# Kernel tuning notes

Measured on AMD Instinct MI355X. Metric: run time of the kernel, lower is better.

Reference implementation:

```python
import jax, jax.numpy as jnp
import numpy as np

WS = 8  # window size
NH = 6  # num heads


def _rel_pos_index(ws):
    coords = jnp.stack(jnp.meshgrid(jnp.arange(ws), jnp.arange(ws), indexing='ij'))  # (2, ws, ws)
    cf = coords.reshape(2, -1)                      # (2, ws*ws)
    rel = cf[:, :, None] - cf[:, None, :]           # (2, ws2, ws2)
    return (rel[0] + ws - 1) * (2 * ws - 1) + (rel[1] + ws - 1)  # (ws2, ws2) int


def setup_inputs() -> dict:
    key = jax.random.key(0)
    k1, k2, k3, k4, k5 = jax.random.split(key, 5)
    B, H, W, C = 4, 256, 256, 192
    dim = C
    x = jax.random.normal(k1, (B, H * W, C), dtype=jnp.float32)
    qkv_w = jax.random.normal(k2, (3 * dim, dim), dtype=jnp.float32) * (dim ** -0.5)
    proj_w = jax.random.normal(k3, (dim, dim), dtype=jnp.float32) * (dim ** -0.5)
    proj_b = jax.random.normal(k4, (dim,), dtype=jnp.float32) * 0.01
    rpb_table = jax.random.normal(k5, ((2 * WS - 1) ** 2, NH), dtype=jnp.float32) * 0.02
    return {"x": x, "qkv_w": qkv_w, "proj_w": proj_w, "proj_b": proj_b,
            "rpb_table": rpb_table, "H": H, "W": W}


def reference(x, qkv_w, proj_w, proj_b, rpb_table, H, W):
    B, L, C = x.shape
    ws, nh = WS, NH
    hd = C // nh
    scale = hd ** -0.5
    ws2 = ws * ws

    pad_r = (ws - W % ws) % ws
    pad_b = (ws - H % ws) % ws
    Hp, Wp = H + pad_b, W + pad_r
    xi = x.reshape(B, H, W, C)
    if pad_r > 0 or pad_b > 0:
        xi = jnp.pad(xi, ((0, 0), (0, pad_b), (0, pad_r), (0, 0)))

    # window partition -> (nW, ws2, C)
    win = xi.reshape(B, Hp // ws, ws, Wp // ws, ws, C)
    win = win.transpose(0, 1, 3, 2, 4, 5).reshape(-1, ws2, C)

    # qkv projection (no bias)
    qkv = (win @ qkv_w.T).reshape(-1, ws2, 3, nh, hd)
    q = qkv[:, :, 0].transpose(0, 2, 1, 3) * scale  # (nW, nh, ws2, hd)
    k = qkv[:, :, 1].transpose(0, 2, 1, 3)
    v = qkv[:, :, 2].transpose(0, 2, 1, 3)

    attn = jnp.einsum('nhqd,nhkd->nhqk', q, k)      # (nW, nh, ws2, ws2)
    bias = rpb_table[_rel_pos_index(ws)]            # (ws2, ws2, nh)
    attn = attn + bias.transpose(2, 0, 1)[None]
    attn = jax.nn.softmax(attn, axis=-1)

    out = jnp.einsum('nhqk,nhkd->nhqd', attn, v)    # (nW, nh, ws2, hd)
    out = out.transpose(0, 2, 1, 3).reshape(-1, ws2, C)
    out = out @ proj_w.T + proj_b

    # window reverse
    xo = out.reshape(B, Hp // ws, Wp // ws, ws, ws, C)
    xo = xo.transpose(0, 1, 3, 2, 4, 5).reshape(B, Hp, Wp, C)
    if pad_r > 0 or pad_b > 0:
        xo = xo[:, :H, :W, :]
    return xo.reshape(B, H * W, C)
```

## Files before the change

### kernel.cpp

```cpp
#include <hip/hip_runtime.h>

typedef _Float16 f16;
typedef _Float16 f16x8 __attribute__((ext_vector_type(8)));
typedef _Float16 f16x4 __attribute__((ext_vector_type(4)));
typedef __fp16 h16x2 __attribute__((ext_vector_type(2)));
typedef float f32x4 __attribute__((ext_vector_type(4)));

constexpr int HDIM = 256, WDIM = 256, C_ = 192, NH_ = 6;
constexpr float SCALE = 0.17677669529663687f;
constexpr int XP = 200;

#define SCHED_FENCE() __builtin_amdgcn_sched_barrier(0)

constexpr size_t OFF_WQ   = 0;
constexpr size_t OFF_WP   = 221184;
constexpr size_t OFF_BIAS = 294912;

__global__ __launch_bounds__(256) void prep_kernel(const float* __restrict__ qkv_w,
                                                   const float* __restrict__ proj_w,
                                                   const float* __restrict__ rpb,
                                                   f16* __restrict__ wqp, f16* __restrict__ wpp,
                                                   f16* __restrict__ biasp) {
    int i = blockIdx.x * 256 + threadIdx.x;
    if (i < 13824) {
        int lane = i & 63, rest = i >> 6;
        int ks = rest % 6; rest /= 6;
        int dt = rest & 1; rest >>= 1;
        int c = rest % 3, w = rest / 3;
        int l15 = lane & 15, lg = lane >> 4;
        int row = c * 192 + w * 32 + dt * 16 + l15;
        int col = ks * 32 + lg * 8;
#pragma unroll
        for (int j = 0; j < 8; ++j) wqp[(size_t)i * 8 + j] = (f16)qkv_w[row * 192 + col + j];
    } else if (i < 18432) {
        int g = i - 13824;
        int lane = g & 63, rest = g >> 6;
        int ks = rest % 6; rest /= 6;
        int nt = rest & 1, w = rest >> 1;
        int l15 = lane & 15, lg = lane >> 4;
        int row = w * 32 + nt * 16 + l15;
        int col = ks * 32 + lg * 8;
#pragma unroll
        for (int j = 0; j < 8; ++j) wpp[(size_t)g * 8 + j] = (f16)proj_w[row * 192 + col + j];
    } else if (i < 24576) {
        int g = i - 18432;
        int lane = g & 63;
        int kt = (g >> 6) & 3, qt = (g >> 8) & 3, h = g >> 10;
        int q = qt * 16 + (lane & 15);
#pragma unroll
        for (int j = 0; j < 4; ++j) {
            int k = kt * 16 + (lane >> 4) * 4 + j;
            int dy = (q >> 3) - (k >> 3) + 7;
            int dx = (q & 7) - (k & 7) + 7;
            biasp[(size_t)g * 4 + j] = (f16)rpb[(dy * 15 + dx) * NH_ + h];
        }
    }
}

__global__ __launch_bounds__(128, 2) void fused_kernel(const float* __restrict__ x,
                                                       const f16* __restrict__ wqp,
                                                       const f16* __restrict__ wpp,
                                                       const float* __restrict__ pb,
                                                       const f16* __restrict__ biasp,
                                                       float* __restrict__ out) {
    __shared__ f16 xlds[64 * XP];
    const int tid = threadIdx.x;
    const int v = tid >> 6;
    const int lane = tid & 63;
    const int l15 = lane & 15, lg = lane >> 4;
    const int win = blockIdx.x;
    const int b = win >> 10, wy = (win >> 5) & 31, wx = win & 31;

#pragma unroll
    for (int it = 0; it < 24; ++it) {
        int u = tid + it * 128;
        int row = u / 48, c4 = u - row * 48;
        int gy = wy * 8 + (row >> 3), gx = wx * 8 + (row & 7);
        float4 vv = *((const float4*)(x + ((size_t)((b * HDIM + gy) * WDIM + gx)) * C_ + c4 * 4));
        h16x2 p0 = __builtin_amdgcn_cvt_pkrtz(vv.x, vv.y);
        h16x2 p1 = __builtin_amdgcn_cvt_pkrtz(vv.z, vv.w);
        f16x4 o4;
        o4[0] = (f16)p0[0]; o4[1] = (f16)p0[1]; o4[2] = (f16)p1[0]; o4[3] = (f16)p1[1];
        *((f16x4*)(xlds + row * XP + c4 * 4)) = o4;
    }
    SCHED_FENCE();
    __syncthreads();

    f16x4 oreg[3][4][2];

#pragma unroll
    for (int hh = 0; hh < 3; ++hh) {
        const int head = v * 3 + hh;
        const f16x8* wqb   = (const f16x8*)wqp + (size_t)head * 36 * 64 + lane;
        const f16x4* bbase = (const f16x4*)biasp + (size_t)head * 16 * 64 + lane;
        SCHED_FENCE();

        f16x4 qf[2][4], kf[2][4];
        {
            f32x4 aq[2][4], ak[2][4];
#pragma unroll
            for (int ii = 0; ii < 4; ++ii)
#pragma unroll
                for (int jj = 0; jj < 2; ++jj) {
                    f32x4 z = {0.f, 0.f, 0.f, 0.f};
                    aq[jj][ii] = z; ak[jj][ii] = z;
                }
#pragma unroll
            for (int ks = 0; ks < 6; ++ks) {
                f16x8 Wq0 = wqb[(size_t)(     ks) * 64], Wq1 = wqb[(size_t)( 6 + ks) * 64];
                f16x8 Wk0 = wqb[(size_t)(12 + ks) * 64], Wk1 = wqb[(size_t)(18 + ks) * 64];
#pragma unroll
                for (int tt = 0; tt < 4; ++tt) {
                    f16x8 xt = *((const f16x8*)(xlds + (tt * 16 + l15) * XP + ks * 32 + lg * 8));
                    aq[0][tt] = __builtin_amdgcn_mfma_f32_16x16x32_f16(Wq0, xt, aq[0][tt], 0, 0, 0);
                    aq[1][tt] = __builtin_amdgcn_mfma_f32_16x16x32_f16(Wq1, xt, aq[1][tt], 0, 0, 0);
                    ak[0][tt] = __builtin_amdgcn_mfma_f32_16x16x32_f16(Wk0, xt, ak[0][tt], 0, 0, 0);
                    ak[1][tt] = __builtin_amdgcn_mfma_f32_16x16x32_f16(Wk1, xt, ak[1][tt], 0, 0, 0);
                }
            }
#pragma unroll
            for (int dt = 0; dt < 2; ++dt)
#pragma unroll
                for (int tt = 0; tt < 4; ++tt)
#pragma unroll
                    for (int ii = 0; ii < 4; ++ii) {
                        qf[dt][tt][ii] = (f16)(aq[dt][tt][ii] * SCALE);
                        kf[dt][tt][ii] = (f16)(ak[dt][tt][ii]);
                    }
        }
        SCHED_FENCE();

        f16x4 vf[4][2];
        {
            f32x4 av[4][2];
#pragma unroll
            for (int ii = 0; ii < 4; ++ii)
#pragma unroll
                for (int jj = 0; jj < 2; ++jj) {
                    f32x4 z = {0.f, 0.f, 0.f, 0.f};
                    av[ii][jj] = z;
                }
#pragma unroll
            for (int ks = 0; ks < 6; ++ks) {
                f16x8 Wv0 = wqb[(size_t)(24 + ks) * 64], Wv1 = wqb[(size_t)(30 + ks) * 64];
#pragma unroll
                for (int tt = 0; tt < 4; ++tt) {
                    f16x8 xt = *((const f16x8*)(xlds + (tt * 16 + l15) * XP + ks * 32 + lg * 8));
                    av[tt][0] = __builtin_amdgcn_mfma_f32_16x16x32_f16(xt, Wv0, av[tt][0], 0, 0, 0);
                    av[tt][1] = __builtin_amdgcn_mfma_f32_16x16x32_f16(xt, Wv1, av[tt][1], 0, 0, 0);
                }
            }
#pragma unroll
            for (int tt = 0; tt < 4; ++tt)
#pragma unroll
                for (int dt = 0; dt < 2; ++dt)
#pragma unroll
                    for (int ii = 0; ii < 4; ++ii)
                        vf[tt][dt][ii] = (f16)(av[tt][dt][ii]);
        }
        SCHED_FENCE();

#pragma unroll
        for (int qt = 0; qt < 4; ++qt) {
            f16x4 bq[4];
#pragma unroll
            for (int kt = 0; kt < 4; ++kt)
                bq[kt] = bbase[(size_t)(qt * 4 + kt) * 64];
            f32x4 s[4];
#pragma unroll
            for (int kt = 0; kt < 4; ++kt) {
                f32x4 z = {0.f, 0.f, 0.f, 0.f};
                s[kt] = __builtin_amdgcn_mfma_f32_16x16x16f16(kf[0][kt], qf[0][qt], z, 0, 0, 0);
                s[kt] = __builtin_amdgcn_mfma_f32_16x16x16f16(kf[1][kt], qf[1][qt], s[kt], 0, 0, 0);
            }
#pragma unroll
            for (int kt = 0; kt < 4; ++kt)
#pragma unroll
                for (int ii = 0; ii < 4; ++ii) s[kt][ii] += (float)bq[kt][ii];

            float m = s[0][0];
#pragma unroll
            for (int kt = 0; kt < 4; ++kt)
#pragma unroll
                for (int ii = 0; ii < 4; ++ii) m = fmaxf(m, s[kt][ii]);
            m = fmaxf(m, __shfl_xor(m, 16));
            m = fmaxf(m, __shfl_xor(m, 32));
            float sum = 0.f;
            f16x4 pa[4];
#pragma unroll
            for (int kt = 0; kt < 4; ++kt)
#pragma unroll
                for (int ii = 0; ii < 4; ++ii) {
                    float e = __expf(s[kt][ii] - m);
                    sum += e;
                    pa[kt][ii] = (f16)e;
                }
            sum += __shfl_xor(sum, 16);
            sum += __shfl_xor(sum, 32);
            const float rq = 1.0f / sum;

#pragma unroll
            for (int dt = 0; dt < 2; ++dt) {
                f32x4 z = {0.f, 0.f, 0.f, 0.f};
                f32x4 o0 = __builtin_amdgcn_mfma_f32_16x16x16f16(vf[0][dt], pa[0], z, 0, 0, 0);
                o0 = __builtin_amdgcn_mfma_f32_16x16x16f16(vf[1][dt], pa[1], o0, 0, 0, 0);
                f32x4 o1 = __builtin_amdgcn_mfma_f32_16x16x16f16(vf[2][dt], pa[2], z, 0, 0, 0);
                o1 = __builtin_amdgcn_mfma_f32_16x16x16f16(vf[3][dt], pa[3], o1, 0, 0, 0);
                f32x4 o = o0 + o1;
                f16x4 ov;
#pragma unroll
                for (int ii = 0; ii < 4; ++ii) ov[ii] = (f16)(o[ii] * rq);
                oreg[hh][qt][dt] = ov;
            }
        }
    }
    SCHED_FENCE();
    __syncthreads();

#pragma unroll
    for (int hh = 0; hh < 3; ++hh) {
        const int head = v * 3 + hh;
#pragma unroll
        for (int qt = 0; qt < 4; ++qt)
#pragma unroll
            for (int dt = 0; dt < 2; ++dt)
                *((f16x4*)(xlds + (qt * 16 + l15) * XP + head * 32 + dt * 16 + lg * 4)) = oreg[hh][qt][dt];
    }
    SCHED_FENCE();
    __syncthreads();

#pragma unroll
    for (int hh = 0; hh < 3; ++hh) {
        const int head = v * 3 + hh;
        const f16x8* wpb = (const f16x8*)wpp + (size_t)head * 12 * 64 + lane;
#pragma unroll
        for (int nt = 0; nt < 2; ++nt) {
            f16x8 wpf[6];
#pragma unroll
            for (int ks = 0; ks < 6; ++ks)
                wpf[ks] = wpb[(size_t)(nt * 6 + ks) * 64];
            f32x4 bv = *((const f32x4*)(pb + head * 32 + nt * 16 + lg * 4));
#pragma unroll
            for (int qt = 0; qt < 4; ++qt) {
                f32x4 acc = {0.f, 0.f, 0.f, 0.f};
#pragma unroll
                for (int ks = 0; ks < 6; ++ks) {
                    f16x8 af = *((const f16x8*)(xlds + (qt * 16 + l15) * XP + ks * 32 + lg * 8));
                    acc = __builtin_amdgcn_mfma_f32_16x16x32_f16(wpf[ks], af, acc, 0, 0, 0);
                }
                acc += bv;
                const int t = qt * 16 + l15;
                const int gy = wy * 8 + (t >> 3), gx = wx * 8 + (t & 7);
                *((f32x4*)(out + ((size_t)((b * HDIM + gy) * WDIM + gx)) * C_ + head * 32 + nt * 16 + lg * 4)) = acc;
            }
        }
    }
}

extern "C" void kernel_launch(void* const* d_in, const int* in_sizes, int n_in,
                              void* d_out, int out_size, void* d_ws, size_t ws_size,
                              hipStream_t stream) {
    const float* x      = (const float*)d_in[0];
    const float* qkv_w  = (const float*)d_in[1];
    const float* proj_w = (const float*)d_in[2];
    const float* proj_b = (const float*)d_in[3];
    const float* rpb    = (const float*)d_in[4];
    float* out = (float*)d_out;
    char* ws = (char*)d_ws;
    f16* wqp   = (f16*)(ws + OFF_WQ);
    f16* wpp   = (f16*)(ws + OFF_WP);
    f16* biasp = (f16*)(ws + OFF_BIAS);

    prep_kernel<<<96, 256, 0, stream>>>(qkv_w, proj_w, rpb, wqp, wpp, biasp);
    fused_kernel<<<4096, 128, 0, stream>>>(x, wqp, wpp, proj_b, biasp, out);
}
```

Before: 172.6 us.

## Fold scale and log2e into weights, seed MFMA with fp32 bias, raise occupancy

Folds the attention scale and log2(e) into the Q weights and the relative-position bias during prep, so softmax can use raw v_exp_f32 and a hardware reciprocal. The bias is stored in fp32 and passed as the MFMA accumulator seed, which removes the separate bias add. Launch bounds go from 2 to 3 blocks per SIMD, and the x load loop is split into three scheduling groups. The higher occupancy target may force register spills, and the fp32 bias doubles that table's memory traffic.

```diff
diff --git a/kernel.cpp b/kernel.cpp
--- a/kernel.cpp
+++ b/kernel.cpp
@@ -8,6 +8,8 @@
 
 constexpr int HDIM = 256, WDIM = 256, C_ = 192, NH_ = 6;
 constexpr float SCALE = 0.17677669529663687f;
+constexpr float L2E = 1.4426950408889634f;
+constexpr float SCALE2 = SCALE * L2E;
 constexpr int XP = 200;
 
 #define SCHED_FENCE() __builtin_amdgcn_sched_barrier(0)
@@ -20,7 +22,7 @@
                                                    const float* __restrict__ proj_w,
                                                    const float* __restrict__ rpb,
                                                    f16* __restrict__ wqp, f16* __restrict__ wpp,
-                                                   f16* __restrict__ biasp) {
+                                                   float* __restrict__ biasp) {
     int i = blockIdx.x * 256 + threadIdx.x;
     if (i < 13824) {
         int lane = i & 63, rest = i >> 6;
@@ -30,8 +32,9 @@
         int l15 = lane & 15, lg = lane >> 4;
         int row = c * 192 + w * 32 + dt * 16 + l15;
         int col = ks * 32 + lg * 8;
-#pragma unroll
-        for (int j = 0; j < 8; ++j) wqp[(size_t)i * 8 + j] = (f16)qkv_w[row * 192 + col + j];
+        float sc = (c == 0) ? SCALE2 : 1.0f;
+#pragma unroll
+        for (int j = 0; j < 8; ++j) wqp[(size_t)i * 8 + j] = (f16)(qkv_w[row * 192 + col + j] * sc);
     } else if (i < 18432) {
         int g = i - 13824;
         int lane = g & 63, rest = g >> 6;
@@ -52,16 +55,16 @@
             int k = kt * 16 + (lane >> 4) * 4 + j;
             int dy = (q >> 3) - (k >> 3) + 7;
             int dx = (q & 7) - (k & 7) + 7;
-            biasp[(size_t)g * 4 + j] = (f16)rpb[(dy * 15 + dx) * NH_ + h];
+            biasp[(size_t)g * 4 + j] = rpb[(dy * 15 + dx) * NH_ + h] * L2E;
         }
     }
 }
 
-__global__ __launch_bounds__(128, 2) void fused_kernel(const float* __restrict__ x,
+__global__ __launch_bounds__(128, 3) void fused_kernel(const float* __restrict__ x,
                                                        const f16* __restrict__ wqp,
                                                        const f16* __restrict__ wpp,
                                                        const float* __restrict__ pb,
-                                                       const f16* __restrict__ biasp,
+                                                       const float* __restrict__ biasp,
                                                        float* __restrict__ out) {
     __shared__ f16 xlds[64 * XP];
     const int tid = threadIdx.x;
@@ -72,18 +75,21 @@
     const int b = win >> 10, wy = (win >> 5) & 31, wx = win & 31;
 
 #pragma unroll
-    for (int it = 0; it < 24; ++it) {
-        int u = tid + it * 128;
-        int row = u / 48, c4 = u - row * 48;
-        int gy = wy * 8 + (row >> 3), gx = wx * 8 + (row & 7);
-        float4 vv = *((const float4*)(x + ((size_t)((b * HDIM + gy) * WDIM + gx)) * C_ + c4 * 4));
-        h16x2 p0 = __builtin_amdgcn_cvt_pkrtz(vv.x, vv.y);
-        h16x2 p1 = __builtin_amdgcn_cvt_pkrtz(vv.z, vv.w);
-        f16x4 o4;
-        o4[0] = (f16)p0[0]; o4[1] = (f16)p0[1]; o4[2] = (f16)p1[0]; o4[3] = (f16)p1[1];
-        *((f16x4*)(xlds + row * XP + c4 * 4)) = o4;
-    }
-    SCHED_FENCE();
+    for (int grp = 0; grp < 3; ++grp) {
+#pragma unroll
+        for (int it8 = 0; it8 < 8; ++it8) {
+            int u = tid + (grp * 8 + it8) * 128;
+            int row = u / 48, c4 = u - row * 48;
+            int gy = wy * 8 + (row >> 3), gx = wx * 8 + (row & 7);
+            float4 vv = *((const float4*)(x + ((size_t)((b * HDIM + gy) * WDIM + gx)) * C_ + c4 * 4));
+            h16x2 p0 = __builtin_amdgcn_cvt_pkrtz(vv.x, vv.y);
+            h16x2 p1 = __builtin_amdgcn_cvt_pkrtz(vv.z, vv.w);
+            f16x4 o4;
+            o4[0] = (f16)p0[0]; o4[1] = (f16)p0[1]; o4[2] = (f16)p1[0]; o4[3] = (f16)p1[1];
+            *((f16x4*)(xlds + row * XP + c4 * 4)) = o4;
+        }
+        SCHED_FENCE();
+    }
     __syncthreads();
 
     f16x4 oreg[3][4][2];
@@ -92,7 +98,7 @@
     for (int hh = 0; hh < 3; ++hh) {
         const int head = v * 3 + hh;
         const f16x8* wqb   = (const f16x8*)wqp + (size_t)head * 36 * 64 + lane;
-        const f16x4* bbase = (const f16x4*)biasp + (size_t)head * 16 * 64 + lane;
+        const f32x4* bbase = (const f32x4*)biasp + (size_t)head * 16 * 64 + lane;
         SCHED_FENCE();
 
         f16x4 qf[2][4], kf[2][4];
@@ -124,7 +130,7 @@
                 for (int tt = 0; tt < 4; ++tt)
 #pragma unroll
                     for (int ii = 0; ii < 4; ++ii) {
-                        qf[dt][tt][ii] = (f16)(aq[dt][tt][ii] * SCALE);
+                        qf[dt][tt][ii] = (f16)(aq[dt][tt][ii]);
                         kf[dt][tt][ii] = (f16)(ak[dt][tt][ii]);
                     }
         }
@@ -136,18 +142,15 @@
 #pragma unroll
             for (int ii = 0; ii < 4; ++ii)
 #pragma unroll
-                for (int jj = 0; jj < 2; ++jj) {
-                    f32x4 z = {0.f, 0.f, 0.f, 0.f};
-                    av[ii][jj] = z;
-                }
+                for (int jj = 0; jj < 2; ++jj) { f32x4 z = {0.f,0.f,0.f,0.f}; av[ii][jj] = z; }
 #pragma unroll
             for (int ks = 0; ks < 6; ++ks) {
-                f16x8 Wv0 = wqb[(size_t)(24 + ks) * 64], Wv1 = wqb[(size_t)(30 + ks) * 64];
+                f16x8 W0 = wqb[(size_t)(24 + ks) * 64], W1 = wqb[(size_t)(30 + ks) * 64];
 #pragma unroll
                 for (int tt = 0; tt < 4; ++tt) {
                     f16x8 xt = *((const f16x8*)(xlds + (tt * 16 + l15) * XP + ks * 32 + lg * 8));
-                    av[tt][0] = __builtin_amdgcn_mfma_f32_16x16x32_f16(xt, Wv0, av[tt][0], 0, 0, 0);
-                    av[tt][1] = __builtin_amdgcn_mfma_f32_16x16x32_f16(xt, Wv1, av[tt][1], 0, 0, 0);
+                    av[tt][0] = __builtin_amdgcn_mfma_f32_16x16x32_f16(xt, W0, av[tt][0], 0, 0, 0);
+                    av[tt][1] = __builtin_amdgcn_mfma_f32_16x16x32_f16(xt, W1, av[tt][1], 0, 0, 0);
                 }
             }
 #pragma unroll
@@ -162,22 +165,13 @@
 
 #pragma unroll
         for (int qt = 0; qt < 4; ++qt) {
-            f16x4 bq[4];
-#pragma unroll
-            for (int kt = 0; kt < 4; ++kt)
-                bq[kt] = bbase[(size_t)(qt * 4 + kt) * 64];
             f32x4 s[4];
 #pragma unroll
             for (int kt = 0; kt < 4; ++kt) {
-                f32x4 z = {0.f, 0.f, 0.f, 0.f};
-                s[kt] = __builtin_amdgcn_mfma_f32_16x16x16f16(kf[0][kt], qf[0][qt], z, 0, 0, 0);
+                f32x4 bb = bbase[(size_t)(qt * 4 + kt) * 64];
+                s[kt] = __builtin_amdgcn_mfma_f32_16x16x16f16(kf[0][kt], qf[0][qt], bb, 0, 0, 0);
                 s[kt] = __builtin_amdgcn_mfma_f32_16x16x16f16(kf[1][kt], qf[1][qt], s[kt], 0, 0, 0);
             }
-#pragma unroll
-            for (int kt = 0; kt < 4; ++kt)
-#pragma unroll
-                for (int ii = 0; ii < 4; ++ii) s[kt][ii] += (float)bq[kt][ii];
-
             float m = s[0][0];
 #pragma unroll
             for (int kt = 0; kt < 4; ++kt)
@@ -191,13 +185,14 @@
             for (int kt = 0; kt < 4; ++kt)
 #pragma unroll
                 for (int ii = 0; ii < 4; ++ii) {
-                    float e = __expf(s[kt][ii] - m);
+                    float e;
+                    asm("v_exp_f32 %0, %1" : "=v"(e) : "v"(s[kt][ii] - m));
                     sum += e;
                     pa[kt][ii] = (f16)e;
                 }
             sum += __shfl_xor(sum, 16);
             sum += __shfl_xor(sum, 32);
-            const float rq = 1.0f / sum;
+            const float rq = __builtin_amdgcn_rcpf(sum);
 
 #pragma unroll
             for (int dt = 0; dt < 2; ++dt) {
@@ -267,9 +262,9 @@
     const float* rpb    = (const float*)d_in[4];
     float* out = (float*)d_out;
     char* ws = (char*)d_ws;
-    f16* wqp   = (f16*)(ws + OFF_WQ);
-    f16* wpp   = (f16*)(ws + OFF_WP);
-    f16* biasp = (f16*)(ws + OFF_BIAS);
+    f16* wqp     = (f16*)(ws + OFF_WQ);
+    f16* wpp     = (f16*)(ws + OFF_WP);
+    float* biasp = (float*)(ws + OFF_BIAS);
 
     prep_kernel<<<96, 256, 0, stream>>>(qkv_w, proj_w, rpb, wqp, wpp, biasp);
     fused_kernel<<<4096, 128, 0, stream>>>(x, wqp, wpp, proj_b, biasp, out);
```

After: 176.0 us. About the same (+2.0%).
